# Kernel optimization log

Hardware: AMD Instinct MI355X
Metric: run time of the kernel (lower is better)

## Reference

```python
import jax, jax.numpy as jnp
import numpy as np

N = 100000      # nodes
E = 1600000     # edges
IN_DIM = 128
OUT_DIM = 128
H = 8           # num_heads
D = OUT_DIM // H  # per-head dim = 16
L = 2           # num_layers
NEG_SLOPE = 0.1


def setup_inputs() -> dict:
    key = jax.random.key(0)
    ks = jax.random.split(key, 12)
    features = jax.random.normal(ks[0], (N, IN_DIM), dtype=jnp.float32)
    src = jax.random.randint(ks[1], (E,), 0, N, dtype=jnp.int32)
    dst = jax.random.randint(ks[2], (E,), 0, N, dtype=jnp.int32)
    w = jax.random.uniform(ks[3], (E,), dtype=jnp.float32)
    # per-layer params: fc weight [in, H*D], attn_left/right [H, D]
    s = 1.0 / np.sqrt(IN_DIM)
    W1 = jax.random.uniform(ks[4], (IN_DIM, H * D), minval=-s, maxval=s, dtype=jnp.float32)
    al1 = jax.random.normal(ks[5], (H, D), dtype=jnp.float32) * 0.1
    ar1 = jax.random.normal(ks[6], (H, D), dtype=jnp.float32) * 0.1
    W2 = jax.random.uniform(ks[7], (OUT_DIM, H * D), minval=-s, maxval=s, dtype=jnp.float32)
    al2 = jax.random.normal(ks[8], (H, D), dtype=jnp.float32) * 0.1
    ar2 = jax.random.normal(ks[9], (H, D), dtype=jnp.float32) * 0.1
    so = 1.0 / np.sqrt(L * OUT_DIM)
    Wm = jax.random.uniform(ks[10], (L * OUT_DIM, OUT_DIM), minval=-so, maxval=so, dtype=jnp.float32)
    bm = jax.random.uniform(ks[11], (OUT_DIM,), minval=-so, maxval=so, dtype=jnp.float32)
    return {"features": features, "src": src, "dst": dst, "w": w,
            "W1": W1, "al1": al1, "ar1": ar1, "W2": W2, "al2": al2, "ar2": ar2,
            "Wm": Wm, "bm": bm}


def gat_layer(x, src, dst, w, W, al, ar):
    # x: [N, in_dim] -> ft: [N, H, D]
    ft = (x @ W).reshape(N, H, D)
    el = jnp.einsum('nhd,hd->nh', ft, al)  # [N, H]
    er = jnp.einsum('nhd,hd->nh', ft, ar)  # [N, H]
    # edge-wise u_add_v + leaky_relu, scaled by edge weight w
    e = jax.nn.leaky_relu(el[src] + er[dst], negative_slope=NEG_SLOPE)  # [E, H]
    e = w[:, None] * e
    # edge_softmax over incoming edges of each dst node (numerically stable)
    m = jax.ops.segment_max(e, dst, num_segments=N)  # [N, H]
    m = jnp.where(jnp.isfinite(m), m, 0.0)           # empty segments -> 0
    ex = jnp.exp(e - m[dst])
    s = jax.ops.segment_sum(ex, dst, num_segments=N)  # [N, H] (>0 wherever indexed)
    a = ex / s[dst]                                   # [E, H]
    # u_mul_e + sum aggregation
    msg = ft[src] * a[:, :, None]                     # [E, H, D]
    out = jax.ops.segment_sum(msg, dst, num_segments=N)  # [N, H, D]
    out = jax.nn.relu(out)
    return out.reshape(N, H * D)  # concat heads


def reference(features, src, dst, w, W1, al1, ar1, W2, al2, ar2, Wm, bm):
    x1 = gat_layer(features, src, dst, w, W1, al1, ar1)
    x2 = gat_layer(x1, src, dst, w, W2, al2, ar2)
    h = jnp.concatenate([x1, x2], axis=-1)  # [N, L*OUT_DIM]
    return h @ Wm + bm                       # [N, OUT_DIM]
```

## Files before the change

kernel.cpp:

```cpp
#include <hip/hip_runtime.h>
#include <hip/hip_bf16.h>

#define NEG_SLOPE 0.1f
#define EPB 4096
#define BINSH 9

typedef __attribute__((ext_vector_type(8))) short bf16x8;
typedef __attribute__((ext_vector_type(4))) float f32x4;

__device__ __forceinline__ float bf2f(unsigned u) { return __uint_as_float(u << 16); }
__device__ __forceinline__ unsigned short f2bf(float f) {
    __hip_bfloat16 h = __float2bfloat16(f);
    unsigned short r;
    __builtin_memcpy(&r, &h, 2);
    return r;
}

__global__ __launch_bounds__(256) void binhist_k(const int* __restrict__ dst,
                                                 int* __restrict__ bin_counts, int E) {
    __shared__ int cnt[256];
    int t = threadIdx.x;
    cnt[t] = 0;
    __syncthreads();
    int base = blockIdx.x * EPB;
    if (base + EPB <= E) {
        const int4* d4 = (const int4*)(dst + base);
        #pragma unroll
        for (int i = 0; i < 4; ++i) {
            int4 v = d4[i * 256 + t];
            atomicAdd(&cnt[v.x >> BINSH], 1);
            atomicAdd(&cnt[v.y >> BINSH], 1);
            atomicAdd(&cnt[v.z >> BINSH], 1);
            atomicAdd(&cnt[v.w >> BINSH], 1);
        }
    } else {
        for (int i = 0; i < 4; ++i) {
            int j0 = base + (i * 256 + t) * 4;
            #pragma unroll
            for (int c = 0; c < 4; ++c)
                if (j0 + c < E) atomicAdd(&cnt[dst[j0 + c] >> BINSH], 1);
        }
    }
    __syncthreads();
    if (cnt[t]) atomicAdd(&bin_counts[t], cnt[t]);
}

__global__ __launch_bounds__(256) void scan256_k(const int* __restrict__ bin_counts,
                                                 int* __restrict__ binoffs,
                                                 int* __restrict__ gcur, int nbins) {
    __shared__ int sbuf[256];
    int t = threadIdx.x;
    int c = (t < nbins) ? bin_counts[t] : 0;
    sbuf[t] = c;
    __syncthreads();
    for (int off = 1; off < 256; off <<= 1) {
        int u = (t >= off) ? sbuf[t - off] : 0;
        __syncthreads();
        sbuf[t] += u;
        __syncthreads();
    }
    int ex = sbuf[t] - c;
    binoffs[t] = ex;
    if (t == 255) binoffs[256] = ex + c;
    gcur[t] = ex;
}

__global__ __launch_bounds__(256) void binify_k(const int* __restrict__ src,
                                                const int* __restrict__ dst,
                                                const float* __restrict__ w,
                                                int* __restrict__ gcur,
                                                int4* __restrict__ tmp, int E) {
    __shared__ int cnt[256];
    __shared__ int basearr[256];
    int t = threadIdx.x;
    cnt[t] = 0;
    __syncthreads();
    int base = blockIdx.x * EPB;
    int es[16], ed[16], ew[16];
    bool va[16];
    if (base + EPB <= E) {
        const int4* s4 = (const int4*)(src + base);
        const int4* d4 = (const int4*)(dst + base);
        const int4* w4 = (const int4*)(w + base);
        #pragma unroll
        for (int i = 0; i < 4; ++i) {
            int slot = i * 256 + t;
            int4 sv = s4[slot]; int4 dv = d4[slot]; int4 wv = w4[slot];
            es[i*4+0]=sv.x; es[i*4+1]=sv.y; es[i*4+2]=sv.z; es[i*4+3]=sv.w;
            ed[i*4+0]=dv.x; ed[i*4+1]=dv.y; ed[i*4+2]=dv.z; ed[i*4+3]=dv.w;
            ew[i*4+0]=wv.x; ew[i*4+1]=wv.y; ew[i*4+2]=wv.z; ew[i*4+3]=wv.w;
            va[i*4+0]=va[i*4+1]=va[i*4+2]=va[i*4+3]=true;
        }
    } else {
        #pragma unroll
        for (int i = 0; i < 4; ++i) {
            #pragma unroll
            for (int c = 0; c < 4; ++c) {
                int j = base + (i * 256 + t) * 4 + c;
                bool v = j < E;
                va[i*4+c] = v;
                es[i*4+c] = v ? src[j] : 0;
                ed[i*4+c] = v ? dst[j] : 0;
                ew[i*4+c] = v ? __float_as_int(w[j]) : 0;
            }
        }
    }
    #pragma unroll
    for (int i = 0; i < 16; ++i)
        if (va[i]) atomicAdd(&cnt[ed[i] >> BINSH], 1);
    __syncthreads();
    int c = cnt[t];
    basearr[t] = c ? atomicAdd(&gcur[t], c) : 0;
    __syncthreads();
    cnt[t] = 0;
    __syncthreads();
    #pragma unroll
    for (int i = 0; i < 16; ++i) {
        if (va[i]) {
            int b = ed[i] >> BINSH;
            int pos = atomicAdd(&cnt[b], 1);
            tmp[basearr[b] + pos] = make_int4(es[i], ew[i], ed[i], 0);
        }
    }
}

__global__ __launch_bounds__(256) void binfin_k(const int4* __restrict__ tmp,
                                                const int* __restrict__ binoffs,
                                                int* __restrict__ offs,
                                                int2* __restrict__ snw, int N, int E) {
    __shared__ int ncnt[512];
    __shared__ int noff[512];
    __shared__ int sbuf[256];
    int b = blockIdx.x, t = threadIdx.x;
    int lo = b << BINSH;
    int hi = min(lo + 512, N);
    int ebeg = binoffs[b], eend = binoffs[b + 1];
    ncnt[t] = 0; ncnt[t + 256] = 0;
    __syncthreads();
    for (int j = ebeg + t; j < eend; j += 256)
        atomicAdd(&ncnt[tmp[j].z - lo], 1);
    __syncthreads();
    int a0 = ncnt[2 * t], a1 = ncnt[2 * t + 1];
    sbuf[t] = a0 + a1;
    __syncthreads();
    for (int off = 1; off < 256; off <<= 1) {
        int u = (t >= off) ? sbuf[t - off] : 0;
        __syncthreads();
        sbuf[t] += u;
        __syncthreads();
    }
    int ex = sbuf[t] - (a0 + a1);
    noff[2 * t] = ex;
    noff[2 * t + 1] = ex + a0;
    if (lo + 2 * t     < hi) offs[lo + 2 * t]     = ebeg + ex;
    if (lo + 2 * t + 1 < hi) offs[lo + 2 * t + 1] = ebeg + ex + a0;
    if (b == 0 && t == 0) offs[N] = E;
    ncnt[t] = 0; ncnt[t + 256] = 0;
    __syncthreads();
    for (int j = ebeg + t; j < eend; j += 256) {
        int4 e = tmp[j];
        int idx = e.z - lo;
        int pos = atomicAdd(&ncnt[idx], 1);
        snw[ebeg + noff[idx] + pos] = make_int2(e.x, e.y);
    }
}

__global__ void prep_w_k(const float* __restrict__ W1, const float* __restrict__ W2,
                         const float* __restrict__ Wm, unsigned short* __restrict__ Wt1,
                         unsigned short* __restrict__ Wt2, unsigned short* __restrict__ Wtm) {
    int id = blockIdx.x * blockDim.x + threadIdx.x;
    if (id < 16384) {
        int k = id >> 7, c = id & 127;
        Wt1[c * 128 + k] = f2bf(W1[id]);
    } else if (id < 32768) {
        int e = id - 16384; int k = e >> 7, c = e & 127;
        Wt2[c * 128 + k] = f2bf(W2[e]);
    } else if (id < 65536) {
        int e = id - 32768;
        int k = e >> 7, c = e & 127;
        Wtm[c * 256 + k] = f2bf(Wm[e]);
    }
}

template<int K, bool A_F32, bool BIAS, bool OUT_BF16>
__global__ __launch_bounds__(256) void gemm_mfma(const void* __restrict__ A0v,
                                                 const void* __restrict__ A1v,
                                                 const unsigned short* __restrict__ Wt,
                                                 const float* __restrict__ bias,
                                                 void* __restrict__ Cv, int M) {
    __shared__ __align__(16) unsigned short At[128 * 128];
    __shared__ __align__(16) unsigned short Bt[128 * 128];
    const int t = threadIdx.x;
    const int lane = t & 63;
    const int wv = t >> 6;
    const int m0 = blockIdx.x * 128;
    const int l15 = lane & 15;
    const int l4 = lane >> 4;

    f32x4 acc[2][8];
    #pragma unroll
    for (int r = 0; r < 2; ++r)
        #pragma unroll
        for (int c = 0; c < 8; ++c) acc[r][c] = (f32x4){0.f, 0.f, 0.f, 0.f};

    const int srow = t >> 4;
    const int scol = (t & 15) * 8;

    for (int k0 = 0; k0 < K; k0 += 128) {
        const int chunk = k0 >> 7;
        #pragma unroll
        for (int p = 0; p < 8; ++p) {
            int row = p * 16 + srow;
            int gm = m0 + row;
            uint4 pk = make_uint4(0, 0, 0, 0);
            if (A_F32) {
                const float* Ap = (const float*)(chunk ? A1v : A0v);
                float4 f0 = make_float4(0.f,0.f,0.f,0.f), f1 = f0;
                if (gm < M) {
                    f0 = *(const float4*)(Ap + (size_t)gm * 128 + scol);
                    f1 = *(const float4*)(Ap + (size_t)gm * 128 + scol + 4);
                }
                pk.x = f2bf(f0.x) | ((unsigned)f2bf(f0.y) << 16);
                pk.y = f2bf(f0.z) | ((unsigned)f2bf(f0.w) << 16);
                pk.z = f2bf(f1.x) | ((unsigned)f2bf(f1.y) << 16);
                pk.w = f2bf(f1.z) | ((unsigned)f2bf(f1.w) << 16);
            } else {
                const unsigned short* Ap = (const unsigned short*)(chunk ? A1v : A0v);
                if (gm < M) pk = *(const uint4*)(Ap + (size_t)gm * 128 + scol);
            }
            int byte = (row * 256 + scol * 2) ^ ((row & 7) << 4);
            *(uint4*)((char*)At + byte) = pk;
        }
        #pragma unroll
        for (int p = 0; p < 8; ++p) {
            int row = p * 16 + srow;
            uint4 pk = *(const uint4*)(Wt + (size_t)row * K + k0 + scol);
            int byte = (row * 256 + scol * 2) ^ ((row & 7) << 4);
            *(uint4*)((char*)Bt + byte) = pk;
        }
        __syncthreads();
        #pragma unroll
        for (int ks = 0; ks < 4; ++ks) {
            int kb = ks * 32 + l4 * 8;
            bf16x8 af[2], bfv[8];
            #pragma unroll
            for (int r = 0; r < 2; ++r) {
                int row = wv * 32 + r * 16 + l15;
                int byte = (row * 256 + kb * 2) ^ ((row & 7) << 4);
                af[r] = *(const bf16x8*)((char*)At + byte);
            }
            #pragma unroll
            for (int c = 0; c < 8; ++c) {
                int col = c * 16 + l15;
                int byte = (col * 256 + kb * 2) ^ ((col & 7) << 4);
                bfv[c] = *(const bf16x8*)((char*)Bt + byte);
            }
            #pragma unroll
            for (int r = 0; r < 2; ++r)
                #pragma unroll
                for (int c = 0; c < 8; ++c)
                    acc[r][c] = __builtin_amdgcn_mfma_f32_16x16x32_bf16(af[r], bfv[c], acc[r][c], 0, 0, 0);
        }
        __syncthreads();
    }
    float bb[8];
    if (BIAS) {
        #pragma unroll
        for (int c = 0; c < 8; ++c) bb[c] = bias[c * 16 + l15];
    }
    #pragma unroll
    for (int r = 0; r < 2; ++r) {
        #pragma unroll
        for (int q = 0; q < 4; ++q) {
            int row = m0 + wv * 32 + r * 16 + l4 * 4 + q;
            if (row < M) {
                #pragma unroll
                for (int c = 0; c < 8; ++c) {
                    int col = c * 16 + l15;
                    float v = acc[r][c][q];
                    if (BIAS) v += bb[c];
                    if (OUT_BF16) ((unsigned short*)Cv)[(size_t)row * 128 + col] = f2bf(v);
                    else          ((float*)Cv)[(size_t)row * 128 + col] = v;
                }
            }
        }
    }
}

__global__ void elr_k(const __hip_bfloat16* __restrict__ ft, const float* __restrict__ al,
                      const float* __restrict__ ar, __hip_bfloat16* __restrict__ el,
                      __hip_bfloat16* __restrict__ er, int n) {
    int idx = blockIdx.x * blockDim.x + threadIdx.x;
    if (idx >= n * 8) return;
    int node = idx >> 3, h = idx & 7;
    const __hip_bfloat16* f = ft + (size_t)node * 128 + h * 16;
    uint4 a = *(const uint4*)f;
    uint4 b = *(const uint4*)(f + 8);
    float fv[16];
    fv[0]  = bf2f(a.x & 0xffff); fv[1]  = bf2f(a.x >> 16);
    fv[2]  = bf2f(a.y & 0xffff); fv[3]  = bf2f(a.y >> 16);
    fv[4]  = bf2f(a.z & 0xffff); fv[5]  = bf2f(a.z >> 16);
    fv[6]  = bf2f(a.w & 0xffff); fv[7]  = bf2f(a.w >> 16);
    fv[8]  = bf2f(b.x & 0xffff); fv[9]  = bf2f(b.x >> 16);
    fv[10] = bf2f(b.y & 0xffff); fv[11] = bf2f(b.y >> 16);
    fv[12] = bf2f(b.z & 0xffff); fv[13] = bf2f(b.z >> 16);
    fv[14] = bf2f(b.w & 0xffff); fv[15] = bf2f(b.w >> 16);
    float e1 = 0.f, e2 = 0.f;
    #pragma unroll
    for (int d = 0; d < 16; ++d) { e1 += fv[d] * al[h * 16 + d]; e2 += fv[d] * ar[h * 16 + d]; }
    unsigned short r1 = f2bf(e1), r2 = f2bf(e2);
    __builtin_memcpy(&el[idx], &r1, 2);
    __builtin_memcpy(&er[idx], &r2, 2);
}

__global__ __launch_bounds__(256) void agg_k(const __hip_bfloat16* __restrict__ ftb,
                                             const __hip_bfloat16* __restrict__ el,
                                             const __hip_bfloat16* __restrict__ er,
                                             const int2* __restrict__ snw,
                                             const int* __restrict__ offs,
                                             unsigned short* __restrict__ out, int n) {
    __shared__ int2 rec[4][8][65];
    int wid = threadIdx.x >> 6;
    int node = blockIdx.x * 4 + (threadIdx.x >> 6);
    if (node >= n) return;
    int lane = threadIdx.x & 63;
    int g8 = lane >> 3;
    unsigned lane4 = (unsigned)(lane * 4);
    int beg = offs[node], end = offs[node + 1];
    int deg = end - beg;
    const char* fb = (const char*)ftb;

    float erv[8];
    {
        uint4 u = *(const uint4*)(er + (size_t)node * 8);
        erv[0] = bf2f(u.x & 0xffff); erv[1] = bf2f(u.x >> 16);
        erv[2] = bf2f(u.y & 0xffff); erv[3] = bf2f(u.y >> 16);
        erv[4] = bf2f(u.z & 0xffff); erv[5] = bf2f(u.z >> 16);
        erv[6] = bf2f(u.w & 0xffff); erv[7] = bf2f(u.w >> 16);
    }

    float acc0 = 0.f, acc1 = 0.f, s = 0.f;

    for (int c0 = 0; c0 < deg; c0 += 64) {
        int cnt = min(64, deg - c0);
        if (lane < cnt) {
            int2 p2 = snw[beg + c0 + lane];
            int off = p2.x << 8;
            float wv = __int_as_float(p2.y);
            uint4 u = *(const uint4*)(el + (size_t)p2.x * 8);
            float elv[8];
            elv[0] = bf2f(u.x & 0xffff); elv[1] = bf2f(u.x >> 16);
            elv[2] = bf2f(u.y & 0xffff); elv[3] = bf2f(u.y >> 16);
            elv[4] = bf2f(u.z & 0xffff); elv[5] = bf2f(u.z >> 16);
            elv[6] = bf2f(u.w & 0xffff); elv[7] = bf2f(u.w >> 16);
            #pragma unroll
            for (int h = 0; h < 8; ++h) {
                float tt = elv[h] + erv[h];
                tt = tt > 0.f ? tt : NEG_SLOPE * tt;
                float p = __expf(tt * wv);
                rec[wid][h][lane] = make_int2(off, __float_as_int(p));
            }
        }
        __builtin_amdgcn_wave_barrier();
        asm volatile("s_waitcnt lgkmcnt(0)" ::: "memory");
        __builtin_amdgcn_wave_barrier();

        #pragma unroll 4
        for (int j = 0; j < cnt; ++j) {
            int2 r = rec[wid][g8][j];
            float a = __int_as_float(r.y);
            unsigned vo = (unsigned)r.x + lane4;
            unsigned u = *(const unsigned*)(fb + vo);
            s += a;
            acc0 += a * bf2f(u & 0xffff);
            acc1 += a * bf2f(u >> 16);
        }
        __builtin_amdgcn_wave_barrier();
    }

    float sinv = s > 0.f ? 1.f / s : 0.f;
    float o0 = fmaxf(acc0 * sinv, 0.f);
    float o1 = fmaxf(acc1 * sinv, 0.f);
    unsigned pk = f2bf(o0) | ((unsigned)f2bf(o1) << 16);
    *(unsigned*)(out + (size_t)node * 128 + lane * 2) = pk;
}

extern "C" void kernel_launch(void* const* d_in, const int* in_sizes, int n_in,
                              void* d_out, int out_size, void* d_ws, size_t ws_size,
                              hipStream_t stream) {
    const float* features = (const float*)d_in[0];
    const int*   src      = (const int*)d_in[1];
    const int*   dst      = (const int*)d_in[2];
    const float* w        = (const float*)d_in[3];
    const float* W1       = (const float*)d_in[4];
    const float* al1      = (const float*)d_in[5];
    const float* ar1      = (const float*)d_in[6];
    const float* W2       = (const float*)d_in[7];
    const float* al2      = (const float*)d_in[8];
    const float* ar2      = (const float*)d_in[9];
    const float* Wm       = (const float*)d_in[10];
    const float* bm       = (const float*)d_in[11];
    float* out = (float*)d_out;

    const int N = in_sizes[0] / 128;
    const int E = in_sizes[1];

    char* ws = (char*)d_ws;
    unsigned short* ftb = (unsigned short*)ws;            ws += (size_t)N * 128 * 2;
    unsigned short* x1b = (unsigned short*)ws;            ws += (size_t)N * 128 * 2;
    unsigned short* x2b = (unsigned short*)ws;            ws += (size_t)N * 128 * 2;
    unsigned short* el  = (unsigned short*)ws;            ws += (size_t)N * 8 * 2;
    unsigned short* er  = (unsigned short*)ws;            ws += (size_t)N * 8 * 2;
    unsigned short* Wt1 = (unsigned short*)ws;            ws += (size_t)128 * 128 * 2;
    unsigned short* Wt2 = (unsigned short*)ws;            ws += (size_t)128 * 128 * 2;
    unsigned short* Wtm = (unsigned short*)ws;            ws += (size_t)128 * 256 * 2;
    int* offs      = (int*)ws;                            ws += (size_t)(N + 4) * 4;
    int* bin_counts= (int*)ws;                            ws += 256 * 4;
    int* binoffs   = (int*)ws;                            ws += 260 * 4;
    int* gcur      = (int*)ws;                            ws += 256 * 4;
    int2* snw      = (int2*)ws;                           ws += (size_t)E * 8;
    int4* tmp = (int4*)x1b;

    hipMemsetAsync(bin_counts, 0, 256 * sizeof(int), stream);

    const int nbins = (N + 511) >> BINSH;
    const int nblk_e = (E + EPB - 1) / EPB;

    prep_w_k<<<256, 256, 0, stream>>>(W1, W2, Wm, Wt1, Wt2, Wtm);

    binhist_k<<<nblk_e, 256, 0, stream>>>(dst, bin_counts, E);
    scan256_k<<<1, 256, 0, stream>>>(bin_counts, binoffs, gcur, nbins);
    binify_k<<<nblk_e, 256, 0, stream>>>(src, dst, w, gcur, tmp, E);
    binfin_k<<<nbins, 256, 0, stream>>>(tmp, binoffs, offs, snw, N, E);

    int gemm_grid = (N + 127) / 128;
    int agg_grid = (N + 3) / 4;

    gemm_mfma<128, true, false, true><<<gemm_grid, 256, 0, stream>>>(features, nullptr, Wt1, nullptr, ftb, N);
    elr_k<<<(N * 8 + 255) / 256, 256, 0, stream>>>((const __hip_bfloat16*)ftb, al1, ar1,
                                                   (__hip_bfloat16*)el, (__hip_bfloat16*)er, N);
    agg_k<<<agg_grid, 256, 0, stream>>>((const __hip_bfloat16*)ftb, (const __hip_bfloat16*)el,
                                        (const __hip_bfloat16*)er, snw, offs, x1b, N);

    gemm_mfma<128, false, false, true><<<gemm_grid, 256, 0, stream>>>(x1b, nullptr, Wt2, nullptr, ftb, N);
    elr_k<<<(N * 8 + 255) / 256, 256, 0, stream>>>((const __hip_bfloat16*)ftb, al2, ar2,
                                                   (__hip_bfloat16*)el, (__hip_bfloat16*)er, N);
    agg_k<<<agg_grid, 256, 0, stream>>>((const __hip_bfloat16*)ftb, (const __hip_bfloat16*)el,
                                        (const __hip_bfloat16*)er, snw, offs, x2b, N);

    gemm_mfma<256, false, true, false><<<gemm_grid, 256, 0, stream>>>(x1b, x2b, Wtm, bm, out, N);
}
```

Measured before the change: 295.3 us.

## Process four degree-sorted nodes per wavefront in GAT aggregation

The aggregation kernel now packs four destination nodes into each 64-lane wavefront, 16 lanes per node, each lane loading 16 bytes of features and keeping eight accumulators. Nodes are first counting-sorted by in-degree into a permutation, so nodes sharing a wavefront have similar degrees and fewer lanes sit idle. This targets the poor lane use of one-node-per-wave with an average degree of 16, at the cost of three extra small kernels and scattered output writes. It also swaps the bf16 high-half unpack for a mask instead of a shift.

```diff
diff --git a/kernel.cpp b/kernel.cpp
--- a/kernel.cpp
+++ b/kernel.cpp
@@ -4,11 +4,14 @@
 #define NEG_SLOPE 0.1f
 #define EPB 4096
 #define BINSH 9
+#define DMAX 512
 
 typedef __attribute__((ext_vector_type(8))) short bf16x8;
 typedef __attribute__((ext_vector_type(4))) float f32x4;
 
 __device__ __forceinline__ float bf2f(unsigned u) { return __uint_as_float(u << 16); }
+__device__ __forceinline__ float bflo(unsigned u) { return __uint_as_float(u << 16); }
+__device__ __forceinline__ float bfhi(unsigned u) { return __uint_as_float(u & 0xffff0000u); }
 __device__ __forceinline__ unsigned short f2bf(float f) {
     __hip_bfloat16 h = __float2bfloat16(f);
     unsigned short r;
@@ -162,6 +165,48 @@
         int idx = e.z - lo;
         int pos = atomicAdd(&ncnt[idx], 1);
         snw[ebeg + noff[idx] + pos] = make_int2(e.x, e.y);
+    }
+}
+
+__global__ __launch_bounds__(256) void deghist_k(const int* __restrict__ offs,
+                                                 int* __restrict__ dhist, int N) {
+    __shared__ int h[DMAX];
+    int t = threadIdx.x;
+    for (int i = t; i < DMAX; i += 256) h[i] = 0;
+    __syncthreads();
+    int n = blockIdx.x * 256 + t;
+    if (n < N) {
+        int d = min(offs[n + 1] - offs[n], DMAX - 1);
+        atomicAdd(&h[d], 1);
+    }
+    __syncthreads();
+    for (int i = t; i < DMAX; i += 256) if (h[i]) atomicAdd(&dhist[i], h[i]);
+}
+
+__global__ __launch_bounds__(512) void degscan_k(const int* __restrict__ dhist,
+                                                 int* __restrict__ dcur) {
+    __shared__ int buf[DMAX];
+    int t = threadIdx.x;
+    int v = dhist[t];
+    buf[t] = v;
+    __syncthreads();
+    for (int off = 1; off < DMAX; off <<= 1) {
+        int u = (t >= off) ? buf[t - off] : 0;
+        __syncthreads();
+        buf[t] += u;
+        __syncthreads();
+    }
+    dcur[t] = buf[t] - v;
+}
+
+__global__ __launch_bounds__(256) void degscat_k(const int* __restrict__ offs,
+                                                 int* __restrict__ dcur,
+                                                 int* __restrict__ perm, int N) {
+    int n = blockIdx.x * 256 + threadIdx.x;
+    if (n < N) {
+        int d = min(offs[n + 1] - offs[n], DMAX - 1);
+        int pos = atomicAdd(&dcur[d], 1);
+        perm[pos] = n;
     }
 }
 
@@ -297,14 +342,14 @@
     uint4 a = *(const uint4*)f;
     uint4 b = *(const uint4*)(f + 8);
     float fv[16];
-    fv[0]  = bf2f(a.x & 0xffff); fv[1]  = bf2f(a.x >> 16);
-    fv[2]  = bf2f(a.y & 0xffff); fv[3]  = bf2f(a.y >> 16);
-    fv[4]  = bf2f(a.z & 0xffff); fv[5]  = bf2f(a.z >> 16);
-    fv[6]  = bf2f(a.w & 0xffff); fv[7]  = bf2f(a.w >> 16);
-    fv[8]  = bf2f(b.x & 0xffff); fv[9]  = bf2f(b.x >> 16);
-    fv[10] = bf2f(b.y & 0xffff); fv[11] = bf2f(b.y >> 16);
-    fv[12] = bf2f(b.z & 0xffff); fv[13] = bf2f(b.z >> 16);
-    fv[14] = bf2f(b.w & 0xffff); fv[15] = bf2f(b.w >> 16);
+    fv[0]  = bflo(a.x); fv[1]  = bfhi(a.x);
+    fv[2]  = bflo(a.y); fv[3]  = bfhi(a.y);
+    fv[4]  = bflo(a.z); fv[5]  = bfhi(a.z);
+    fv[6]  = bflo(a.w); fv[7]  = bfhi(a.w);
+    fv[8]  = bflo(b.x); fv[9]  = bfhi(b.x);
+    fv[10] = bflo(b.y); fv[11] = bfhi(b.y);
+    fv[12] = bflo(b.z); fv[13] = bfhi(b.z);
+    fv[14] = bflo(b.w); fv[15] = bfhi(b.w);
     float e1 = 0.f, e2 = 0.f;
     #pragma unroll
     for (int d = 0; d < 16; ++d) { e1 += fv[d] * al[h * 16 + d]; e2 += fv[d] * ar[h * 16 + d]; }
@@ -318,71 +363,96 @@
                                              const __hip_bfloat16* __restrict__ er,
                                              const int2* __restrict__ snw,
                                              const int* __restrict__ offs,
+                                             const int* __restrict__ perm,
                                              unsigned short* __restrict__ out, int n) {
-    __shared__ int2 rec[4][8][65];
+    __shared__ int2 rec[4][16][4][8];
     int wid = threadIdx.x >> 6;
-    int node = blockIdx.x * 4 + (threadIdx.x >> 6);
-    if (node >= n) return;
     int lane = threadIdx.x & 63;
-    int g8 = lane >> 3;
-    unsigned lane4 = (unsigned)(lane * 4);
-    int beg = offs[node], end = offs[node + 1];
-    int deg = end - beg;
+    int g = lane >> 4;
+    int gl = lane & 15;
+    int hd = gl >> 1;
+    unsigned gl16 = (unsigned)(gl * 16);
+    int idx = blockIdx.x * 16 + wid * 4 + g;
+    bool valid = idx < n;
+    int node = valid ? perm[idx] : 0;
+    int beg = 0, deg = 0;
+    if (valid) { beg = offs[node]; deg = offs[node + 1] - beg; }
     const char* fb = (const char*)ftb;
 
     float erv[8];
     {
         uint4 u = *(const uint4*)(er + (size_t)node * 8);
-        erv[0] = bf2f(u.x & 0xffff); erv[1] = bf2f(u.x >> 16);
-        erv[2] = bf2f(u.y & 0xffff); erv[3] = bf2f(u.y >> 16);
-        erv[4] = bf2f(u.z & 0xffff); erv[5] = bf2f(u.z >> 16);
-        erv[6] = bf2f(u.w & 0xffff); erv[7] = bf2f(u.w >> 16);
-    }
-
-    float acc0 = 0.f, acc1 = 0.f, s = 0.f;
-
-    for (int c0 = 0; c0 < deg; c0 += 64) {
-        int cnt = min(64, deg - c0);
-        if (lane < cnt) {
-            int2 p2 = snw[beg + c0 + lane];
+        erv[0] = bflo(u.x); erv[1] = bfhi(u.x);
+        erv[2] = bflo(u.y); erv[3] = bfhi(u.y);
+        erv[4] = bflo(u.z); erv[5] = bfhi(u.z);
+        erv[6] = bflo(u.w); erv[7] = bfhi(u.w);
+    }
+
+    float acc[8];
+    #pragma unroll
+    for (int k = 0; k < 8; ++k) acc[k] = 0.f;
+    float s = 0.f;
+
+    int wdeg = deg;
+    wdeg = max(wdeg, __shfl_xor(wdeg, 16));
+    wdeg = max(wdeg, __shfl_xor(wdeg, 32));
+
+    for (int c0 = 0; c0 < wdeg; c0 += 16) {
+        int cnt = min(16, deg - c0);
+        if (gl < cnt) {
+            int2 p2 = snw[beg + c0 + gl];
             int off = p2.x << 8;
             float wv = __int_as_float(p2.y);
             uint4 u = *(const uint4*)(el + (size_t)p2.x * 8);
             float elv[8];
-            elv[0] = bf2f(u.x & 0xffff); elv[1] = bf2f(u.x >> 16);
-            elv[2] = bf2f(u.y & 0xffff); elv[3] = bf2f(u.y >> 16);
-            elv[4] = bf2f(u.z & 0xffff); elv[5] = bf2f(u.z >> 16);
-            elv[6] = bf2f(u.w & 0xffff); elv[7] = bf2f(u.w >> 16);
+            elv[0] = bflo(u.x); elv[1] = bfhi(u.x);
+            elv[2] = bflo(u.y); elv[3] = bfhi(u.y);
+            elv[4] = bflo(u.z); elv[5] = bfhi(u.z);
+            elv[6] = bflo(u.w); elv[7] = bfhi(u.w);
             #pragma unroll
             for (int h = 0; h < 8; ++h) {
                 float tt = elv[h] + erv[h];
                 tt = tt > 0.f ? tt : NEG_SLOPE * tt;
                 float p = __expf(tt * wv);
-                rec[wid][h][lane] = make_int2(off, __float_as_int(p));
+                rec[wid][gl][g][h ^ (gl & 7)] = make_int2(off, __float_as_int(p));
             }
         }
         __builtin_amdgcn_wave_barrier();
         asm volatile("s_waitcnt lgkmcnt(0)" ::: "memory");
         __builtin_amdgcn_wave_barrier();
 
+        int cmax = cnt;
+        cmax = max(cmax, __shfl_xor(cmax, 16));
+        cmax = max(cmax, __shfl_xor(cmax, 32));
+
         #pragma unroll 4
-        for (int j = 0; j < cnt; ++j) {
-            int2 r = rec[wid][g8][j];
-            float a = __int_as_float(r.y);
-            unsigned vo = (unsigned)r.x + lane4;
-            unsigned u = *(const unsigned*)(fb + vo);
-            s += a;
-            acc0 += a * bf2f(u & 0xffff);
-            acc1 += a * bf2f(u >> 16);
+        for (int j = 0; j < cmax; ++j) {
+            if (j < cnt) {
+                int2 r = rec[wid][j][g][hd ^ (j & 7)];
+                float a = __int_as_float(r.y);
+                uint4 u = *(const uint4*)(fb + ((unsigned)r.x + gl16));
+                s += a;
+                acc[0] += a * bflo(u.x); acc[1] += a * bfhi(u.x);
+                acc[2] += a * bflo(u.y); acc[3] += a * bfhi(u.y);
+                acc[4] += a * bflo(u.z); acc[5] += a * bfhi(u.z);
+                acc[6] += a * bflo(u.w); acc[7] += a * bfhi(u.w);
+            }
         }
         __builtin_amdgcn_wave_barrier();
     }
 
-    float sinv = s > 0.f ? 1.f / s : 0.f;
-    float o0 = fmaxf(acc0 * sinv, 0.f);
-    float o1 = fmaxf(acc1 * sinv, 0.f);
-    unsigned pk = f2bf(o0) | ((unsigned)f2bf(o1) << 16);
-    *(unsigned*)(out + (size_t)node * 128 + lane * 2) = pk;
+    if (valid) {
+        float sinv = s > 0.f ? 1.f / s : 0.f;
+        float o[8];
+        #pragma unroll
+        for (int k = 0; k < 8; ++k) o[k] = fmaxf(acc[k] * sinv, 0.f);
+        uint4 pk;
+        pk.x = f2bf(o[0]) | ((unsigned)f2bf(o[1]) << 16);
+        pk.y = f2bf(o[2]) | ((unsigned)f2bf(o[3]) << 16);
+        pk.z = f2bf(o[4]) | ((unsigned)f2bf(o[5]) << 16);
+        pk.w = f2bf(o[6]) | ((unsigned)f2bf(o[7]) << 16);
+        *(uint4*)((char*)out + (size_t)node * 256 + gl16) = pk;
+    }
 }
 
 extern "C" void kernel_launch(void* const* d_in, const int* in_sizes, int n_in,
@@ -418,13 +488,18 @@
     int* bin_counts= (int*)ws;                            ws += 256 * 4;
     int* binoffs   = (int*)ws;                            ws += 260 * 4;
     int* gcur      = (int*)ws;                            ws += 256 * 4;
+    int* dhist     = (int*)ws;                            ws += DMAX * 4;
+    int* dcur      = (int*)ws;                            ws += DMAX * 4;
+    int* perm      = (int*)ws;                            ws += (size_t)N * 4;
     int2* snw      = (int2*)ws;                           ws += (size_t)E * 8;
     int4* tmp = (int4*)x1b;
 
     hipMemsetAsync(bin_counts, 0, 256 * sizeof(int), stream);
+    hipMemsetAsync(dhist, 0, DMAX * sizeof(int), stream);
 
     const int nbins = (N + 511) >> BINSH;
     const int nblk_e = (E + EPB - 1) / EPB;
+    const int nblk_n = (N + 255) / 256;
 
     prep_w_k<<<256, 256, 0, stream>>>(W1, W2, Wm, Wt1, Wt2, Wtm);
 
@@ -433,20 +508,24 @@
     binify_k<<<nblk_e, 256, 0, stream>>>(src, dst, w, gcur, tmp, E);
     binfin_k<<<nbins, 256, 0, stream>>>(tmp, binoffs, offs, snw, N, E);
 
+    deghist_k<<<nblk_n, 256, 0, stream>>>(offs, dhist, N);
+    degscan_k<<<1, 512, 0, stream>>>(dhist, dcur);
+    degscat_k<<<nblk_n, 256, 0, stream>>>(offs, dcur, perm, N);
+
     int gemm_grid = (N + 127) / 128;
-    int agg_grid = (N + 3) / 4;
+    int agg_grid = (N + 15) / 16;
 
     gemm_mfma<128, true, false, true><<<gemm_grid, 256, 0, stream>>>(features, nullptr, Wt1, nullptr, ftb, N);
     elr_k<<<(N * 8 + 255) / 256, 256, 0, stream>>>((const __hip_bfloat16*)ftb, al1, ar1,
                                                    (__hip_bfloat16*)el, (__hip_bfloat16*)er, N);
     agg_k<<<agg_grid, 256, 0, stream>>>((const __hip_bfloat16*)ftb, (const __hip_bfloat16*)el,
-                                        (const __hip_bfloat16*)er, snw, offs, x1b, N);
+                                        (const __hip_bfloat16*)er, snw, offs, perm, x1b, N);
 
     gemm_mfma<128, false, false, true><<<gemm_grid, 256, 0, stream>>>(x1b, nullptr, Wt2, nullptr, ftb, N);
     elr_k<<<(N * 8 + 255) / 256, 256, 0, stream>>>((const __hip_bfloat16*)ftb, al2, ar2,
                                                    (__hip_bfloat16*)el, (__hip_bfloat16*)er, N);
     agg_k<<<agg_grid, 256, 0, stream>>>((const __hip_bfloat16*)ftb, (const __hip_bfloat16*)el,
-                                        (const __hip_bfloat16*)er, snw, offs, x2b, N);
+                                        (const __hip_bfloat16*)er, snw, offs, perm, x2b, N);
 
     gemm_mfma<256, false, true, false><<<gemm_grid, 256, 0, stream>>>(x1b, x2b, Wtm, bm, out, N);
 }
```

Result: slower. 602.3 us (+104.0%).
